# Optimization experiments

Hardware: AMD Instinct MI355X
Metric: run time of the kernel (lower is better)

## Reference

```python
import jax, jax.numpy as jnp
import numpy as np

DIM = 256
HEADS = 8
WS = 8      # window size
SS = 4      # shift size
EPS = 1e-5
HEAD_DIM = DIM // HEADS
SCALE = HEAD_DIM ** (-0.5)
N = WS * WS

# relative position index, replicating tf.meshgrid default 'xy' indexing
_ch = np.arange(WS)
_coords = np.stack(np.meshgrid(_ch, _ch, indexing='xy'))          # [2, WS, WS]
_flat = _coords.reshape(2, -1)                                     # [2, N]
_rel = _flat[:, :, None] - _flat[:, None, :]                       # [2, N, N]
_rel = _rel.transpose(1, 2, 0) + np.array([WS - 1, WS - 1])
_rel = _rel * np.array([2 * WS - 1, 1])
RPI = jnp.asarray(_rel.sum(-1).reshape(-1))                        # [N*N] int


def _calc_mask(H, W):
    # faithful to source: mask is -100 where window region ids are EQUAL, 0 otherwise
    img = np.zeros((H, W))
    slices = (slice(0, -WS), slice(-WS, -SS), slice(-SS, None))
    cnt = 0
    for hs in slices:
        for ws_ in slices:
            img[hs, ws_] = cnt
            cnt += 1
    mw = img.reshape(H // WS, WS, W // WS, WS).transpose(0, 2, 1, 3).reshape(-1, N)
    diff = mw[:, None, :] - mw[:, :, None]
    mask = np.where(diff == 0, -100.0, 0.0).astype(np.float32)     # [nW, N, N]
    return jnp.asarray(mask)


def _layernorm(x, g, b):
    m = jnp.mean(x, axis=-1, keepdims=True)
    v = jnp.mean(jnp.square(x - m), axis=-1, keepdims=True)
    return (x - m) * jax.lax.rsqrt(v + EPS) * g + b


def setup_inputs() -> dict:
    key = jax.random.key(0)
    ks = jax.random.split(key, 8)
    B, L, C = 16, 64 * 64, DIM
    s = 0.02
    return {
        'x': jax.random.normal(ks[0], (B, L, C), jnp.float32),
        'norm1_g': jnp.ones((C,), jnp.float32),
        'norm1_b': jnp.zeros((C,), jnp.float32),
        'qkv_w': jax.random.normal(ks[1], (C, 3 * C), jnp.float32) * s,
        'qkv_b': jnp.zeros((3 * C,), jnp.float32),
        'rpb_table': jax.random.normal(ks[2], ((2 * WS - 1) ** 2, HEADS), jnp.float32) * s,
        'proj_w': jax.random.normal(ks[3], (C, C), jnp.float32) * s,
        'proj_b': jnp.zeros((C,), jnp.float32),
        'norm2_g': jnp.ones((C,), jnp.float32),
        'norm2_b': jnp.zeros((C,), jnp.float32),
        'fc1_w': jax.random.normal(ks[4], (C, 4 * C), jnp.float32) * s,
        'fc1_b': jnp.zeros((4 * C,), jnp.float32),
        'fc2_w': jax.random.normal(ks[5], (4 * C, C), jnp.float32) * s,
        'fc2_b': jnp.zeros((C,), jnp.float32),
        'h': 64,
        'w': 64,
    }


def reference(x, norm1_g, norm1_b, qkv_w, qkv_b, rpb_table, proj_w, proj_b,
              norm2_g, norm2_b, fc1_w, fc1_b, fc2_w, fc2_b, h, w):
    B, L, C = x.shape
    nH, nW = h // WS, w // WS
    nWin = nH * nW
    shortcut = x

    xn = _layernorm(x, norm1_g, norm1_b).reshape(B, h, w, C)
    xn = jnp.roll(xn, shift=(-SS, -SS), axis=(1, 2))                 # cyclic shift
    # window partition -> [B*nWin, N, C]
    xw = xn.reshape(B, nH, WS, nW, WS, C).transpose(0, 1, 3, 2, 4, 5).reshape(B * nWin, N, C)

    qkv = (xw @ qkv_w + qkv_b).reshape(B * nWin, N, 3, HEADS, HEAD_DIM)
    qkv = qkv.transpose(2, 0, 3, 1, 4)                               # [3, B*nWin, H, N, d]
    q, k, v = qkv[0] * SCALE, qkv[1], qkv[2]

    attn = jnp.einsum('bhnd,bhmd->bhnm', q, k)                       # [B*nWin, H, N, N]
    bias = rpb_table[RPI].reshape(N, N, HEADS).transpose(2, 0, 1)    # [H, N, N]
    attn = attn + bias[None]

    mask = _calc_mask(h, w)                                          # [nWin, N, N]
    attn = attn.reshape(B, nWin, HEADS, N, N) + mask[None, :, None]
    attn = jax.nn.softmax(attn, axis=-1).reshape(B * nWin, HEADS, N, N)

    out = jnp.einsum('bhnm,bhmd->bhnd', attn, v)                     # [B*nWin, H, N, d]
    out = out.transpose(0, 2, 1, 3).reshape(B * nWin, N, C)
    out = out @ proj_w + proj_b

    # window reverse + reverse shift
    out = out.reshape(B, nH, nW, WS, WS, C).transpose(0, 1, 3, 2, 4, 5).reshape(B, h, w, C)
    out = jnp.roll(out, shift=(SS, SS), axis=(1, 2)).reshape(B, h * w, C)

    y = shortcut + out
    m = _layernorm(y, norm2_g, norm2_b)
    m = jax.nn.gelu(m @ fc1_w + fc1_b, approximate=False) @ fc2_w + fc2_b
    # faithful to source: final residual reuses the ORIGINAL shortcut, not y
    return shortcut + m
```

## Files before the change

kernel.cpp:

```cpp
#include <hip/hip_runtime.h>
#include <math.h>

typedef __bf16 bf16;
typedef __bf16 bf16x4 __attribute__((ext_vector_type(4)));
typedef __bf16 bf16x8 __attribute__((ext_vector_type(8)));
typedef float f32x4 __attribute__((ext_vector_type(4)));

#define AS1 __attribute__((address_space(1)))
#define AS3 __attribute__((address_space(3)))

__device__ __forceinline__ void gload_lds16(const bf16* g, bf16* l) {
    __builtin_amdgcn_global_load_lds((const AS1 void*)g, (AS3 void*)l, 16, 0, 0);
}

__device__ __forceinline__ float gelu_fast(float v) {
    const float u = 1.5957691216057308f * (v + 0.044715f * v * v * v);
    return v / (1.0f + __expf(-u));
}

__global__ __launch_bounds__(256)
void wprep_all(const float* __restrict__ qkv_w, const float* __restrict__ proj_w,
               const float* __restrict__ fc1_w, const float* __restrict__ fc2_w,
               bf16* __restrict__ qkv_wt, bf16* __restrict__ proj_wt,
               bf16* __restrict__ fc1_wt, bf16* __restrict__ fc2_wt)
{
    int idx = blockIdx.x * 256 + threadIdx.x;
    const float* src; bf16* dst; int K, N;
    if (idx < 196608)            { src = qkv_w;  dst = qkv_wt;  K = 256;  N = 768; }
    else if (idx < 262144)       { idx -= 196608; src = proj_w; dst = proj_wt; K = 256;  N = 256; }
    else if (idx < 524288)       { idx -= 262144; src = fc1_w;  dst = fc1_wt;  K = 256;  N = 1024; }
    else                         { idx -= 524288; src = fc2_w;  dst = fc2_wt;  K = 1024; N = 256; }
    const int k = idx / N, n = idx % N;
    dst[(long)n * K + k] = (bf16)src[idx];
}

__global__ __launch_bounds__(256)
void ln1_window(const float* __restrict__ x, const float* __restrict__ g,
                const float* __restrict__ be, bf16* __restrict__ xw)
{
    const int t = threadIdx.x;
    const int lane = t & 63;
    const int w = t >> 6;
    const long tok = (long)blockIdx.x * 4 + w;
    const float4 v = ((const float4*)(x + tok * 256))[lane];
    float sum = v.x + v.y + v.z + v.w;
    float sq  = v.x * v.x + v.y * v.y + v.z * v.z + v.w * v.w;
#pragma unroll
    for (int m = 32; m >= 1; m >>= 1) {
        sum += __shfl_xor(sum, m, 64);
        sq  += __shfl_xor(sq,  m, 64);
    }
    const float mean = sum * (1.0f / 256.0f);
    const float var  = sq * (1.0f / 256.0f) - mean * mean;
    const float rstd = rsqrtf(var + 1e-5f);
    const float4 gv = ((const float4*)g)[lane];
    const float4 bv = ((const float4*)be)[lane];
    bf16x4 ov;
    ov[0] = (bf16)((v.x - mean) * rstd * gv.x + bv.x);
    ov[1] = (bf16)((v.y - mean) * rstd * gv.y + bv.y);
    ov[2] = (bf16)((v.z - mean) * rstd * gv.z + bv.z);
    ov[3] = (bf16)((v.w - mean) * rstd * gv.w + bv.w);
    const int b = (int)(tok >> 12);
    const int l = (int)(tok & 4095);
    const int i = l >> 6, j = l & 63;
    const int ip = (i + 60) & 63, jp = (j + 60) & 63;
    const int winl = ((ip >> 3) << 3) + (jp >> 3);
    const int n = ((ip & 7) << 3) + (jp & 7);
    const long drow = ((long)b * 64 + winl) * 64 + n;
    *(bf16x4*)(xw + drow * 256 + lane * 4) = ov;
}

__global__ __launch_bounds__(256)
void ln2_kernel(const float* __restrict__ x, const bf16* __restrict__ pj,
                const float* __restrict__ g, const float* __restrict__ be,
                bf16* __restrict__ xn2)
{
    const int t = threadIdx.x;
    const int lane = t & 63;
    const int w = t >> 6;
    const long tok = (long)blockIdx.x * 4 + w;
    const float4 xv = ((const float4*)(x + tok * 256))[lane];
    const bf16x4 pv = *(const bf16x4*)(pj + tok * 256 + lane * 4);
    float y0 = xv.x + (float)pv[0];
    float y1 = xv.y + (float)pv[1];
    float y2 = xv.z + (float)pv[2];
    float y3 = xv.w + (float)pv[3];
    float sum = y0 + y1 + y2 + y3;
    float sq  = y0 * y0 + y1 * y1 + y2 * y2 + y3 * y3;
#pragma unroll
    for (int m = 32; m >= 1; m >>= 1) {
        sum += __shfl_xor(sum, m, 64);
        sq  += __shfl_xor(sq,  m, 64);
    }
    const float mean = sum * (1.0f / 256.0f);
    const float var  = sq * (1.0f / 256.0f) - mean * mean;
    const float rstd = rsqrtf(var + 1e-5f);
    const float4 gv = ((const float4*)g)[lane];
    const float4 bv = ((const float4*)be)[lane];
    bf16x4 ov;
    ov[0] = (bf16)((y0 - mean) * rstd * gv.x + bv.x);
    ov[1] = (bf16)((y1 - mean) * rstd * gv.y + bv.y);
    ov[2] = (bf16)((y2 - mean) * rstd * gv.z + bv.z);
    ov[3] = (bf16)((y3 - mean) * rstd * gv.w + bv.w);
    *(bf16x4*)(xn2 + tok * 256 + lane * 4) = ov;
}

template<int EPI, int KT>
__global__ __launch_bounds__(512, 2)
void gemm_w(const bf16* __restrict__ A, const bf16* __restrict__ Bt,
            const float* __restrict__ bias, void* __restrict__ outp,
            int N, const float* __restrict__ xres, void* __restrict__ aux,
            int gx, int nb)
{
    constexpr int K = KT * 32;
    extern __shared__ bf16 lds[];
    bf16* sA = lds;
    bf16* sB = lds + 3 * 8192;
    const int t = threadIdx.x;
    const int l = t & 63;
    const int w = t >> 6;
    const int wr = w >> 1, wc = w & 1;
    const int q = nb >> 3;
    const int id = ((int)blockIdx.x & 7) * q + ((int)blockIdx.x >> 3);
    const long m0 = (long)(id / gx) * 256;
    const long n0 = (long)(id % gx) * 128;

    const bf16* asrcp[2]; bf16* adstp[2];
#pragma unroll
    for (int j = 0; j < 2; j++) {
        const int idx = j * 512 + t;
        const int p = idx >> 3, s = idx & 7;
        const int sl = s ^ (p & 7);
        const int row = 2 * p + (sl >> 2);
        const int ce = (sl & 3) * 8;
        asrcp[j] = A + (m0 + row) * (long)K + ce;
        adstp[j] = &sA[idx * 8];
    }
    const bf16* bsrcp; bf16* bdstp;
    {
        const int p = t >> 3, s = t & 7;
        const int sl = s ^ (p & 7);
        const int row = 2 * p + (sl >> 2);
        const int ce = (sl & 3) * 8;
        bsrcp = Bt + (n0 + row) * (long)K + ce;
        bdstp = &sB[t * 8];
    }

    const int c = l >> 4;
    int eA[4], eB[4];
#pragma unroll
    for (int i = 0; i < 4; i++) {
        const int rowA = wr * 64 + (l & 15) + i * 16;
        const int pa = rowA >> 1;
        eA[i] = (pa * 8 + ((((rowA & 1) << 2) + c) ^ (pa & 7))) * 8;
        const int rowB = wc * 64 + (l & 15) + i * 16;
        const int pb = rowB >> 1;
        eB[i] = (pb * 8 + ((((rowB & 1) << 2) + c) ^ (pb & 7))) * 8;
    }

    f32x4 acc[4][4];
#pragma unroll
    for (int i = 0; i < 4; i++)
#pragma unroll
        for (int j = 0; j < 4; j++) acc[i][j] = (f32x4){0.f, 0.f, 0.f, 0.f};

#define STAGE(bufi, ko)                                                        \
    do {                                                                       \
        gload_lds16(asrcp[0] + (ko), adstp[0] + (bufi) * 8192);                \
        gload_lds16(asrcp[1] + (ko), adstp[1] + (bufi) * 8192);                \
        gload_lds16(bsrcp + (ko), bdstp + (bufi) * 4096);                      \
    } while (0)

    STAGE(0, 0);
    STAGE(1, 32);

#pragma unroll
    for (int kt = 0; kt < KT; ++kt) {
        const int buf = kt % 3;
        if (kt < KT - 1)
            asm volatile("s_waitcnt vmcnt(3)" ::: "memory");
        else
            asm volatile("s_waitcnt vmcnt(0)" ::: "memory");
        __builtin_amdgcn_s_barrier();
        __builtin_amdgcn_sched_barrier(0);
        if (kt + 2 < KT)
            STAGE((kt + 2) % 3, (kt + 2) * 32);
        bf16x8 av[4], bv[4];
#pragma unroll
        for (int ni = 0; ni < 4; ni++)
            bv[ni] = *(const bf16x8*)&sB[buf * 4096 + eB[ni]];
#pragma unroll
        for (int mi = 0; mi < 4; mi++)
            av[mi] = *(const bf16x8*)&sA[buf * 8192 + eA[mi]];
#pragma unroll
        for (int mi = 0; mi < 4; mi++)
#pragma unroll
            for (int ni = 0; ni < 4; ni++)
                acc[mi][ni] = __builtin_amdgcn_mfma_f32_16x16x32_bf16(
                    bv[ni], av[mi], acc[mi][ni], 0, 0, 0);
    }
#undef STAGE

    const bool transpose_path = (EPI == 2) || (EPI == 0 && n0 < 512);
    if (transpose_path) {
        __syncthreads();
        char* wlds = (char*)(lds) + w * 8704;
#pragma unroll
        for (int mi = 0; mi < 4; mi++)
#pragma unroll
            for (int ni = 0; ni < 4; ni++) {
                const int colb = (ni * 16 + (l >> 4) * 4) * 2;
                const int rowl = mi * 16 + (l & 15);
                const float4 bz = *(const float4*)&bias[n0 + wc * 64 + ni * 16 + (l >> 4) * 4];
                float vv[4];
                vv[0] = acc[mi][ni][0] + bz.x;
                vv[1] = acc[mi][ni][1] + bz.y;
                vv[2] = acc[mi][ni][2] + bz.z;
                vv[3] = acc[mi][ni][3] + bz.w;
                if constexpr (EPI == 2) {
#pragma unroll
                    for (int j = 0; j < 4; j++) vv[j] = gelu_fast(vv[j]);
                }
                bf16x4 ov;
#pragma unroll
                for (int j = 0; j < 4; j++) ov[j] = (bf16)vv[j];
                *(bf16x4*)(wlds + rowl * 136 + (colb ^ ((rowl & 7) << 4))) = ov;
            }
        bf16* outb = (bf16*)outp;
#pragma unroll
        for (int j = 0; j < 8; j++) {
            const int r = j * 8 + (l >> 3);
            const bf16x8 vr = *(const bf16x8*)(wlds + r * 136 + (((l & 7) * 16) ^ ((r & 7) << 4)));
            const long row = m0 + wr * 64 + r;
            const int col = (int)(n0 + wc * 64 + (l & 7) * 8);
            *(bf16x8*)&outb[row * N + col] = vr;
        }
    } else {
#pragma unroll
        for (int mi = 0; mi < 4; mi++)
#pragma unroll
            for (int ni = 0; ni < 4; ni++) {
                const long row = m0 + wr * 64 + mi * 16 + (l & 15);
                const int col = (int)(n0 + wc * 64 + ni * 16 + (l >> 4) * 4);
                const float4 bz = *(const float4*)&bias[col];
                float vv[4];
                vv[0] = acc[mi][ni][0] + bz.x;
                vv[1] = acc[mi][ni][1] + bz.y;
                vv[2] = acc[mi][ni][2] + bz.z;
                vv[3] = acc[mi][ni][3] + bz.w;
                if constexpr (EPI == 3) {
                    const float4 xr = *(const float4*)&xres[row * N + col];
                    float4 ov = {vv[0] + xr.x, vv[1] + xr.y, vv[2] + xr.z, vv[3] + xr.w};
                    *(float4*)&((float*)outp)[row * N + col] = ov;
                } else if constexpr (EPI == 0) {
                    bf16* vt = (bf16*)aux;
                    const int win = (int)(row >> 6);
                    const int n = (int)(row & 63);
#pragma unroll
                    for (int j = 0; j < 4; j++)
                        vt[(long)win * 16384 + (col - 512 + j) * 64 + n] = (bf16)vv[j];
                } else {
                    bf16x4 ov;
#pragma unroll
                    for (int j = 0; j < 4; j++) ov[j] = (bf16)vv[j];
                    if constexpr (EPI == 1) {
                        const int gwin = (int)(row >> 6);
                        const int n = (int)(row & 63);
                        const int bb = gwin >> 6, wi = gwin & 63;
                        const int ipp = ((wi >> 3) << 3) + (n >> 3);
                        const int jpp = ((wi & 7) << 3) + (n & 7);
                        const int ii = (ipp + 4) & 63, jj = (jpp + 4) & 63;
                        const long tok = ((long)bb << 12) + (ii << 6) + jj;
                        *(bf16x4*)&((bf16*)outp)[tok * 256 + col] = ov;
                    } else {
                        *(bf16x4*)&((bf16*)outp)[row * N + col] = ov;
                    }
                }
            }
    }
    (void)xres; (void)aux;
}

__global__ __launch_bounds__(256, 4)
void attn_kernel(const bf16* __restrict__ qkv, const bf16* __restrict__ vT,
                 const float* __restrict__ rpb, bf16* __restrict__ out)
{
    __shared__ bf16 P_lds[4][64 * 64];
    const int t = threadIdx.x;
    const int lane = t & 63;
    const int w = t >> 6;
    const int win = blockIdx.x >> 1;
    const int head = (blockIdx.x & 1) * 4 + w;
    const int wi = win & 63;
    const int lr = lane & 15;
    const int lg = lane >> 4;
    const int lk = lg * 8;
    const long base = (long)win * 64 * 768;
    const float scale = 0.17677669529663687f;
    const int whb = (wi >> 3) << 3;
    const int wwb = (wi & 7) << 3;
    const f32x4 z4 = {0.f, 0.f, 0.f, 0.f};

    const bf16* qp  = qkv + base + head * 32;
    const bf16* kp  = qkv + base + 256 + head * 32;
    const bf16* vtp = vT + (long)win * 16384 + head * 32 * 64;

    int idm[4];
#pragma unroll
    for (int ni = 0; ni < 4; ni++) {
        const int m = ni * 16 + lr;
        const int gi2 = whb + (m >> 3), gj2 = wwb + (m & 7);
        idm[ni] = (gi2 < 56 ? 0 : (gi2 < 60 ? 1 : 2)) * 3 + (gj2 < 56 ? 0 : (gj2 < 60 ? 1 : 2));
    }

    bf16x8 aq[4], bk[4];
#pragma unroll
    for (int mi = 0; mi < 4; mi++)
        aq[mi] = *(const bf16x8*)(qp + (mi * 16 + lr) * 768 + lk);
#pragma unroll
    for (int ni = 0; ni < 4; ni++)
        bk[ni] = *(const bf16x8*)(kp + (ni * 16 + lr) * 768 + lk);

    f32x4 s[4][4];
#pragma unroll
    for (int i = 0; i < 4; i++)
#pragma unroll
        for (int j = 0; j < 4; j++) s[i][j] = z4;
#pragma unroll
    for (int mi = 0; mi < 4; mi++)
#pragma unroll
        for (int ni = 0; ni < 4; ni++)
            s[mi][ni] = __builtin_amdgcn_mfma_f32_16x16x32_bf16(aq[mi], bk[ni], s[mi][ni], 0, 0, 0);

#pragma unroll
    for (int mi = 0; mi < 4; mi++)
#pragma unroll
        for (int r = 0; r < 4; r++) {
            const int n = mi * 16 + lg * 4 + r;
            const int gi = whb + (n >> 3);
            const int gj = wwb + (n & 7);
            const int idn = (gi < 56 ? 0 : (gi < 60 ? 1 : 2)) * 3 + (gj < 56 ? 0 : (gj < 60 ? 1 : 2));
            float vals[4];
            float rowmax = -3.0e38f;
#pragma unroll
            for (int ni = 0; ni < 4; ni++) {
                const int m = ni * 16 + lr;
                const int dj = (n & 7) - (m & 7);
                const int di = (n >> 3) - (m >> 3);
                float sv = s[mi][ni][r] * scale + rpb[((dj + 7) * 15 + (di + 7)) * 8 + head];
                if (idn == idm[ni]) sv -= 100.0f;
                vals[ni] = sv;
                rowmax = fmaxf(rowmax, sv);
            }
#pragma unroll
            for (int msk = 8; msk >= 1; msk >>= 1)
                rowmax = fmaxf(rowmax, __shfl_xor(rowmax, msk, 64));
            float rsum = 0.f;
#pragma unroll
            for (int ni = 0; ni < 4; ni++) {
                const float p = __expf(vals[ni] - rowmax);
                vals[ni] = p;
                rsum += p;
            }
#pragma unroll
            for (int msk = 8; msk >= 1; msk >>= 1)
                rsum += __shfl_xor(rsum, msk, 64);
            const float inv = 1.0f / rsum;
            const int swz = (n & 7) << 3;
#pragma unroll
            for (int ni = 0; ni < 4; ni++)
                P_lds[w][n * 64 + ((ni * 16 + lr) ^ swz)] = (bf16)(vals[ni] * inv);
        }

    f32x4 o[4][2];
#pragma unroll
    for (int i = 0; i < 4; i++)
#pragma unroll
        for (int j = 0; j < 2; j++) o[i][j] = z4;
#pragma unroll
    for (int kk = 0; kk < 2; kk++) {
        bf16x8 bv[2];
#pragma unroll
        for (int ni = 0; ni < 2; ni++)
            bv[ni] = *(const bf16x8*)&vtp[(ni * 16 + lr) * 64 + kk * 32 + lk];
#pragma unroll
        for (int mi = 0; mi < 4; mi++) {
            const int row = mi * 16 + lr;
            const bf16x8 ap = *(const bf16x8*)&P_lds[w][row * 64 + ((kk * 32 + lk) ^ ((row & 7) << 3))];
#pragma unroll
            for (int ni = 0; ni < 2; ni++)
                o[mi][ni] = __builtin_amdgcn_mfma_f32_16x16x32_bf16(bv[ni], ap, o[mi][ni], 0, 0, 0);
        }
    }
#pragma unroll
    for (int mi = 0; mi < 4; mi++)
#pragma unroll
        for (int ni = 0; ni < 2; ni++) {
            const int n = mi * 16 + lr;
            const int d = ni * 16 + lg * 4;
            bf16x4 ov;
            ov[0] = (bf16)o[mi][ni][0]; ov[1] = (bf16)o[mi][ni][1];
            ov[2] = (bf16)o[mi][ni][2]; ov[3] = (bf16)o[mi][ni][3];
            *(bf16x4*)(out + ((long)(win * 64 + n)) * 256 + head * 32 + d) = ov;
        }
}

extern "C" void kernel_launch(void* const* d_in, const int* in_sizes, int n_in,
                              void* d_out, int out_size, void* d_ws, size_t ws_size,
                              hipStream_t stream)
{
    (void)in_sizes; (void)n_in; (void)out_size;
    const float* x      = (const float*)d_in[0];
    const float* n1g    = (const float*)d_in[1];
    const float* n1b    = (const float*)d_in[2];
    const float* qkv_w  = (const float*)d_in[3];
    const float* qkv_b  = (const float*)d_in[4];
    const float* rpb    = (const float*)d_in[5];
    const float* proj_w = (const float*)d_in[6];
    const float* proj_b = (const float*)d_in[7];
    const float* n2g    = (const float*)d_in[8];
    const float* n2b    = (const float*)d_in[9];
    const float* fc1_w  = (const float*)d_in[10];
    const float* fc1_b  = (const float*)d_in[11];
    const float* fc2_w  = (const float*)d_in[12];
    const float* fc2_b  = (const float*)d_in[13];
    float* out = (float*)d_out;

    char* ws = (char*)d_ws;
    bf16* qkv_wt  = (bf16*)(ws + 0);
    bf16* proj_wt = (bf16*)(ws + 393216);
    bf16* fc1_wt  = (bf16*)(ws + 524288);
    bf16* fc2_wt  = (bf16*)(ws + 1048576);
    bf16* xw      = (bf16*)(ws + 2097152);
    bf16* qkvb    = (bf16*)(ws + 35651584);
    bf16* attn_o  = xw;
    bf16* proj_o  = qkvb;
    bf16* vT      = (bf16*)d_out;
    bf16* xn2     = (bf16*)d_out;
    bf16* hbuf    = xw;
    if (ws_size < 136314880ull) return;

    const size_t LB = 73728;

    wprep_all<<<3072, 256, 0, stream>>>(qkv_w, proj_w, fc1_w, fc2_w,
                                        qkv_wt, proj_wt, fc1_wt, fc2_wt);

    ln1_window<<<16384, 256, 0, stream>>>(x, n1g, n1b, xw);
    gemm_w<0, 8><<<1536, 512, LB, stream>>>(xw, qkv_wt, qkv_b, qkvb, 768, nullptr, vT, 6, 1536);
    attn_kernel<<<2048, 256, 0, stream>>>(qkvb, vT, rpb, attn_o);
    gemm_w<1, 8><<<512, 512, LB, stream>>>(attn_o, proj_wt, proj_b, proj_o, 256, nullptr, nullptr, 2, 512);
    ln2_kernel<<<16384, 256, 0, stream>>>(x, proj_o, n2g, n2b, xn2);
    gemm_w<2, 8><<<2048, 512, LB, stream>>>(xn2, fc1_wt, fc1_b, hbuf, 1024, nullptr, nullptr, 8, 2048);
    gemm_w<3, 32><<<512, 512, LB, stream>>>(hbuf, fc2_wt, fc2_b, out, 256, x, nullptr, 2, 512);
}
```

Measured before the change: 284.4 us.

## Fuse fc1+GELU+fc2 MLP into one kernel keeping hidden activations in LDS

```diff
diff --git a/kernel.cpp b/kernel.cpp
--- a/kernel.cpp
+++ b/kernel.cpp
@@ -201,7 +201,7 @@
     }
 #undef STAGE
 
-    const bool transpose_path = (EPI == 2) || (EPI == 0 && n0 < 512);
+    const bool transpose_path = (EPI == 0 && n0 < 512);
     if (transpose_path) {
         __syncthreads();
         char* wlds = (char*)(lds) + w * 8704;
@@ -217,10 +217,6 @@
                 vv[1] = acc[mi][ni][1] + bz.y;
                 vv[2] = acc[mi][ni][2] + bz.z;
                 vv[3] = acc[mi][ni][3] + bz.w;
-                if constexpr (EPI == 2) {
-#pragma unroll
-                    for (int j = 0; j < 4; j++) vv[j] = gelu_fast(vv[j]);
-                }
                 bf16x4 ov;
 #pragma unroll
                 for (int j = 0; j < 4; j++) ov[j] = (bf16)vv[j];
@@ -248,11 +244,7 @@
                 vv[1] = acc[mi][ni][1] + bz.y;
                 vv[2] = acc[mi][ni][2] + bz.z;
                 vv[3] = acc[mi][ni][3] + bz.w;
-                if constexpr (EPI == 3) {
-                    const float4 xr = *(const float4*)&xres[row * N + col];
-                    float4 ov = {vv[0] + xr.x, vv[1] + xr.y, vv[2] + xr.z, vv[3] + xr.w};
-                    *(float4*)&((float*)outp)[row * N + col] = ov;
-                } else if constexpr (EPI == 0) {
+                if constexpr (EPI == 0) {
                     bf16* vt = (bf16*)aux;
                     const int win = (int)(row >> 6);
                     const int n = (int)(row & 63);
@@ -263,22 +255,208 @@
                     bf16x4 ov;
 #pragma unroll
                     for (int j = 0; j < 4; j++) ov[j] = (bf16)vv[j];
-                    if constexpr (EPI == 1) {
-                        const int gwin = (int)(row >> 6);
-                        const int n = (int)(row & 63);
-                        const int bb = gwin >> 6, wi = gwin & 63;
-                        const int ipp = ((wi >> 3) << 3) + (n >> 3);
-                        const int jpp = ((wi & 7) << 3) + (n & 7);
-                        const int ii = (ipp + 4) & 63, jj = (jpp + 4) & 63;
-                        const long tok = ((long)bb << 12) + (ii << 6) + jj;
-                        *(bf16x4*)&((bf16*)outp)[tok * 256 + col] = ov;
-                    } else {
-                        *(bf16x4*)&((bf16*)outp)[row * N + col] = ov;
-                    }
+                    const int gwin = (int)(row >> 6);
+                    const int n = (int)(row & 63);
+                    const int bb = gwin >> 6, wi = gwin & 63;
+                    const int ipp = ((wi >> 3) << 3) + (n >> 3);
+                    const int jpp = ((wi & 7) << 3) + (n & 7);
+                    const int ii = (ipp + 4) & 63, jj = (jpp + 4) & 63;
+                    const long tok = ((long)bb << 12) + (ii << 6) + jj;
+                    *(bf16x4*)&((bf16*)outp)[tok * 256 + col] = ov;
                 }
             }
     }
     (void)xres; (void)aux;
+}
+
+__global__ __launch_bounds__(512, 2)
+void fused_mlp(const bf16* __restrict__ xn2, const bf16* __restrict__ w1t,
+               const bf16* __restrict__ w2t, const float* __restrict__ b1,
+               const float* __restrict__ b2, const float* __restrict__ xres,
+               float* __restrict__ out, int nb)
+{
+    extern __shared__ bf16 lds[];
+    bf16* sX = lds;
+    bf16* sW = lds + 32768;
+    char* sH = (char*)(lds + 32768 + 24576);
+    const int t = threadIdx.x;
+    const int l = t & 63;
+    const int w = t >> 6;
+    const int wr = w >> 2, wc = w & 3;
+    const int q = nb >> 3;
+    const int id = ((int)blockIdx.x & 7) * q + ((int)blockIdx.x >> 3);
+    const long m0 = (long)id * 128;
+
+    const bf16* w1base; bf16* w1dst;
+    {
+        const int p = t >> 3, s = t & 7;
+        const int sl = s ^ (p & 7);
+        const int row = 2 * p + (sl >> 2);
+        const int ce = (sl & 3) * 8;
+        w1base = w1t + (long)row * 256 + ce;
+        w1dst = sW + t * 8;
+    }
+    const bf16* w2base[2]; bf16* w2dst[2];
+#pragma unroll
+    for (int j = 0; j < 2; j++) {
+        const int cc = j * 512 + t;
+        const int p = cc >> 3, s = cc & 7;
+        const int sl = s ^ (p & 7);
+        const int row = 2 * p + (sl >> 2);
+        const int ce = (sl & 3) * 8;
+        w2base[j] = w2t + (long)row * 1024 + ce;
+        w2dst[j] = sW + cc * 8;
+    }
+
+    const int c = l >> 4;
+    int eXA[4], eB1[2], eB2[4], hrA[4], hwOf[4][2];
+#pragma unroll
+    for (int i = 0; i < 4; i++) {
+        const int row = wr * 64 + i * 16 + (l & 15);
+        const int p = row >> 1;
+        eXA[i] = (p * 8 + ((((row & 1) << 2) + c) ^ (p & 7))) * 8;
+        hrA[i] = row * 272 + c * 16;
+#pragma unroll
+        for (int nj = 0; nj < 2; nj++)
+            hwOf[i][nj] = row * 272 + (wc * 32 + nj * 16 + (l >> 4) * 4) * 2;
+    }
+#pragma unroll
+    for (int nj = 0; nj < 2; nj++) {
+        const int brow = wc * 32 + nj * 16 + (l & 15);
+        const int p = brow >> 1;
+        eB1[nj] = (p * 8 + ((((brow & 1) << 2) + c) ^ (p & 7))) * 8;
+    }
+#pragma unroll
+    for (int nj = 0; nj < 4; nj++) {
+        const int brow = wc * 64 + nj * 16 + (l & 15);
+        const int p = brow >> 1;
+        eB2[nj] = (p * 8 + ((((brow & 1) << 2) + c) ^ (p & 7))) * 8;
+    }
+
+    {
+#pragma unroll
+        for (int j = 0; j < 8; j++) {
+            const int idx = j * 512 + t;
+            const int kt = idx >> 9, cc = idx & 511;
+            const int p = cc >> 3, s = cc & 7;
+            const int sl = s ^ (p & 7);
+            const int row = 2 * p + (sl >> 2);
+            const int ce = (sl & 3) * 8;
+            gload_lds16(xn2 + (m0 + row) * 256 + kt * 32 + ce, sX + kt * 4096 + cc * 8);
+        }
+    }
+#define STAGE_P1(hc_, kt_, buf_) \
+    gload_lds16(w1base + (hc_) * 32768 + (kt_) * 32, w1dst + (buf_) * 8192)
+#define STAGE_P2(hc_, kt2_, buf_)                                              \
+    do {                                                                       \
+        gload_lds16(w2base[0] + (hc_) * 128 + (kt2_) * 32, w2dst[0] + (buf_) * 8192); \
+        gload_lds16(w2base[1] + (hc_) * 128 + (kt2_) * 32, w2dst[1] + (buf_) * 8192); \
+    } while (0)
+#define STAGE_G(g_)                                                            \
+    do {                                                                       \
+        if ((g_) < 96) {                                                       \
+            if (((g_) % 12) < 8) STAGE_P1((g_) / 12, (g_) % 12, (g_) % 3);     \
+            else STAGE_P2((g_) / 12, (g_) % 12 - 8, (g_) % 3);                 \
+        }                                                                      \
+    } while (0)
+#define PIPE_WAIT(gn_)                                                         \
+    do {                                                                       \
+        if ((gn_) >= 96)                                                       \
+            asm volatile("s_waitcnt vmcnt(0) lgkmcnt(0)" ::: "memory");        \
+        else if (((gn_) % 12) < 8)                                             \
+            asm volatile("s_waitcnt vmcnt(1) lgkmcnt(0)" ::: "memory");        \
+        else                                                                   \
+            asm volatile("s_waitcnt vmcnt(2) lgkmcnt(0)" ::: "memory");        \
+    } while (0)
+
+    STAGE_P1(0, 0, 0);
+    STAGE_P1(0, 1, 1);
+
+    f32x4 acc[4][4];
+#pragma unroll
+    for (int i = 0; i < 4; i++)
+#pragma unroll
+        for (int j = 0; j < 4; j++) acc[i][j] = (f32x4){0.f, 0.f, 0.f, 0.f};
+
+#pragma unroll
+    for (int hc = 0; hc < 8; hc++) {
+        f32x4 acc1[4][2];
+#pragma unroll
+        for (int i = 0; i < 4; i++)
+#pragma unroll
+            for (int j = 0; j < 2; j++) acc1[i][j] = (f32x4){0.f, 0.f, 0.f, 0.f};
+
+#pragma unroll
+        for (int kt = 0; kt < 8; kt++) {
+            const int g = hc * 12 + kt;
+            PIPE_WAIT(g + 1);
+            __builtin_amdgcn_s_barrier();
+            __builtin_amdgcn_sched_barrier(0);
+            STAGE_G(g + 2);
+            const int buf = g % 3;
+            bf16x8 b0 = *(const bf16x8*)&sW[buf * 8192 + eB1[0]];
+            bf16x8 b1 = *(const bf16x8*)&sW[buf * 8192 + eB1[1]];
+#pragma unroll
+            for (int mi = 0; mi < 4; mi++) {
+                const bf16x8 av = *(const bf16x8*)&sX[kt * 4096 + eXA[mi]];
+                acc1[mi][0] = __builtin_amdgcn_mfma_f32_16x16x32_bf16(b0, av, acc1[mi][0], 0, 0, 0);
+                acc1[mi][1] = __builtin_amdgcn_mfma_f32_16x16x32_bf16(b1, av, acc1[mi][1], 0, 0, 0);
+            }
+        }
+#pragma unroll
+        for (int mi = 0; mi < 4; mi++)
+#pragma unroll
+            for (int nj = 0; nj < 2; nj++) {
+                const int hcol = wc * 32 + nj * 16 + (l >> 4) * 4;
+                const float4 bz = *(const float4*)&b1[hc * 128 + hcol];
+                bf16x4 hv;
+                hv[0] = (bf16)gelu_fast(acc1[mi][nj][0] + bz.x);
+                hv[1] = (bf16)gelu_fast(acc1[mi][nj][1] + bz.y);
+                hv[2] = (bf16)gelu_fast(acc1[mi][nj][2] + bz.z);
+                hv[3] = (bf16)gelu_fast(acc1[mi][nj][3] + bz.w);
+                *(bf16x4*)(sH + hwOf[mi][nj]) = hv;
+            }
+#pragma unroll
+        for (int kt2 = 0; kt2 < 4; kt2++) {
+            const int g = hc * 12 + 8 + kt2;
+            PIPE_WAIT(g + 1);
+            __builtin_amdgcn_s_barrier();
+            __builtin_amdgcn_sched_barrier(0);
+            STAGE_G(g + 2);
+            const int buf = g % 3;
+            bf16x8 bb[4];
+#pragma unroll
+            for (int nj = 0; nj < 4; nj++)
+                bb[nj] = *(const bf16x8*)&sW[buf * 8192 + eB2[nj]];
+#pragma unroll
+            for (int mi = 0; mi < 4; mi++) {
+                const bf16x8 av = *(const bf16x8*)(sH + hrA[mi] + kt2 * 64);
+#pragma unroll
+                for (int nj = 0; nj < 4; nj++)
+                    acc[mi][nj] = __builtin_amdgcn_mfma_f32_16x16x32_bf16(bb[nj], av, acc[mi][nj], 0, 0, 0);
+            }
+        }
+    }
+#undef STAGE_P1
+#undef STAGE_P2
+#undef STAGE_G
+#undef PIPE_WAIT
+
+#pragma unroll
+    for (int mi = 0; mi < 4; mi++)
+#pragma unroll
+        for (int nj = 0; nj < 4; nj++) {
+            const long row = m0 + wr * 64 + mi * 16 + (l & 15);
+            const int col = wc * 64 + nj * 16 + (l >> 4) * 4;
+            const float4 bz = *(const float4*)&b2[col];
+            const float4 xr = *(const float4*)&xres[row * 256 + col];
+            float4 ov;
+            ov.x = acc[mi][nj][0] + bz.x + xr.x;
+            ov.y = acc[mi][nj][1] + bz.y + xr.y;
+            ov.z = acc[mi][nj][2] + bz.z + xr.z;
+            ov.w = acc[mi][nj][3] + bz.w + xr.w;
+            *(float4*)&out[row * 256 + col] = ov;
+        }
 }
 
 __global__ __launch_bounds__(256, 4)
@@ -436,11 +614,11 @@
     bf16* attn_o  = xw;
     bf16* proj_o  = qkvb;
     bf16* vT      = (bf16*)d_out;
-    bf16* xn2     = (bf16*)d_out;
-    bf16* hbuf    = xw;
+    bf16* xn2     = xw;
     if (ws_size < 136314880ull) return;
 
-    const size_t LB = 73728;
+    const size_t LB  = 73728;
+    const size_t LBM = 149504;
 
     wprep_all<<<3072, 256, 0, stream>>>(qkv_w, proj_w, fc1_w, fc2_w,
                                         qkv_wt, proj_wt, fc1_wt, fc2_wt);
@@ -450,6 +628,5 @@
     attn_kernel<<<2048, 256, 0, stream>>>(qkvb, vT, rpb, attn_o);
     gemm_w<1, 8><<<512, 512, LB, stream>>>(attn_o, proj_wt, proj_b, proj_o, 256, nullptr, nullptr, 2, 512);
     ln2_kernel<<<16384, 256, 0, stream>>>(x, proj_o, n2g, n2b, xn2);
-    gemm_w<2, 8><<<2048, 512, LB, stream>>>(xn2, fc1_wt, fc1_b, hbuf, 1024, nullptr, nullptr, 8, 2048);
-    gemm_w<3, 32><<<512, 512, LB, stream>>>(hbuf, fc2_wt, fc2_b, out, 256, x, nullptr, 2, 512);
-}
+    fused_mlp<<<512, 512, LBM, stream>>>(xn2, fc1_wt, fc2_wt, fc1_b, fc2_b, x, out, 512);
+}
```

Result: slower. 331.4 us (+16.5%).

## Fuse projection GEMM with residual add and LayerNorm2 into one kernel

Applied to the files above, without the earlier changes.

```diff
diff --git a/kernel.cpp b/kernel.cpp
--- a/kernel.cpp
+++ b/kernel.cpp
@@ -68,41 +68,6 @@
     const int n = ((ip & 7) << 3) + (jp & 7);
     const long drow = ((long)b * 64 + winl) * 64 + n;
     *(bf16x4*)(xw + drow * 256 + lane * 4) = ov;
-}
-
-__global__ __launch_bounds__(256)
-void ln2_kernel(const float* __restrict__ x, const bf16* __restrict__ pj,
-                const float* __restrict__ g, const float* __restrict__ be,
-                bf16* __restrict__ xn2)
-{
-    const int t = threadIdx.x;
-    const int lane = t & 63;
-    const int w = t >> 6;
-    const long tok = (long)blockIdx.x * 4 + w;
-    const float4 xv = ((const float4*)(x + tok * 256))[lane];
-    const bf16x4 pv = *(const bf16x4*)(pj + tok * 256 + lane * 4);
-    float y0 = xv.x + (float)pv[0];
-    float y1 = xv.y + (float)pv[1];
-    float y2 = xv.z + (float)pv[2];
-    float y3 = xv.w + (float)pv[3];
-    float sum = y0 + y1 + y2 + y3;
-    float sq  = y0 * y0 + y1 * y1 + y2 * y2 + y3 * y3;
-#pragma unroll
-    for (int m = 32; m >= 1; m >>= 1) {
-        sum += __shfl_xor(sum, m, 64);
-        sq  += __shfl_xor(sq,  m, 64);
-    }
-    const float mean = sum * (1.0f / 256.0f);
-    const float var  = sq * (1.0f / 256.0f) - mean * mean;
-    const float rstd = rsqrtf(var + 1e-5f);
-    const float4 gv = ((const float4*)g)[lane];
-    const float4 bv = ((const float4*)be)[lane];
-    bf16x4 ov;
-    ov[0] = (bf16)((y0 - mean) * rstd * gv.x + bv.x);
-    ov[1] = (bf16)((y1 - mean) * rstd * gv.y + bv.y);
-    ov[2] = (bf16)((y2 - mean) * rstd * gv.z + bv.z);
-    ov[3] = (bf16)((y3 - mean) * rstd * gv.w + bv.w);
-    *(bf16x4*)(xn2 + tok * 256 + lane * 4) = ov;
 }
 
 template<int EPI, int KT>
@@ -259,26 +224,175 @@
 #pragma unroll
                     for (int j = 0; j < 4; j++)
                         vt[(long)win * 16384 + (col - 512 + j) * 64 + n] = (bf16)vv[j];
-                } else {
-                    bf16x4 ov;
-#pragma unroll
-                    for (int j = 0; j < 4; j++) ov[j] = (bf16)vv[j];
-                    if constexpr (EPI == 1) {
-                        const int gwin = (int)(row >> 6);
-                        const int n = (int)(row & 63);
-                        const int bb = gwin >> 6, wi = gwin & 63;
-                        const int ipp = ((wi >> 3) << 3) + (n >> 3);
-                        const int jpp = ((wi & 7) << 3) + (n & 7);
-                        const int ii = (ipp + 4) & 63, jj = (jpp + 4) & 63;
-                        const long tok = ((long)bb << 12) + (ii << 6) + jj;
-                        *(bf16x4*)&((bf16*)outp)[tok * 256 + col] = ov;
-                    } else {
-                        *(bf16x4*)&((bf16*)outp)[row * N + col] = ov;
-                    }
                 }
             }
     }
     (void)xres; (void)aux;
+}
+
+__global__ __launch_bounds__(512, 2)
+void proj_ln2(const bf16* __restrict__ A, const bf16* __restrict__ Bt,
+              const float* __restrict__ bias, const float* __restrict__ x,
+              const float* __restrict__ g2, const float* __restrict__ b2,
+              bf16* __restrict__ xn2, int nb)
+{
+    extern __shared__ bf16 lds[];
+    bf16* sA = lds;
+    bf16* sB = lds + 3 * 4096;
+    float* sred = (float*)(lds + 3 * 4096 + 3 * 8192);
+    const int t = threadIdx.x;
+    const int l = t & 63;
+    const int w = t >> 6;
+    const int wr = w >> 2, wc = w & 3;
+    const int q = nb >> 3;
+    const int id = ((int)blockIdx.x & 7) * q + ((int)blockIdx.x >> 3);
+    const long m0 = (long)id * 128;
+
+    const bf16* asrcp; bf16* adstp;
+    {
+        const int p = t >> 3, s = t & 7;
+        const int sl = s ^ (p & 7);
+        const int row = 2 * p + (sl >> 2);
+        const int ce = (sl & 3) * 8;
+        asrcp = A + (m0 + row) * 256 + ce;
+        adstp = &sA[t * 8];
+    }
+    const bf16* bsrcp[2]; bf16* bdstp[2];
+#pragma unroll
+    for (int j = 0; j < 2; j++) {
+        const int idx = j * 512 + t;
+        const int p = idx >> 3, s = idx & 7;
+        const int sl = s ^ (p & 7);
+        const int row = 2 * p + (sl >> 2);
+        const int ce = (sl & 3) * 8;
+        bsrcp[j] = Bt + (long)row * 256 + ce;
+        bdstp[j] = &sB[idx * 8];
+    }
+
+    const int c = l >> 4;
+    int eA[4], eB[4];
+#pragma unroll
+    for (int i = 0; i < 4; i++) {
+        const int rowA = wr * 64 + (l & 15) + i * 16;
+        const int pa = rowA >> 1;
+        eA[i] = (pa * 8 + ((((rowA & 1) << 2) + c) ^ (pa & 7))) * 8;
+        const int rowB = wc * 64 + (l & 15) + i * 16;
+        const int pb = rowB >> 1;
+        eB[i] = (pb * 8 + ((((rowB & 1) << 2) + c) ^ (pb & 7))) * 8;
+    }
+
+    f32x4 acc[4][4];
+#pragma unroll
+    for (int i = 0; i < 4; i++)
+#pragma unroll
+        for (int j = 0; j < 4; j++) acc[i][j] = (f32x4){0.f, 0.f, 0.f, 0.f};
+
+#define STAGE(bufi, ko)                                                        \
+    do {                                                                       \
+        gload_lds16(asrcp + (ko), adstp + (bufi) * 4096);                      \
+        gload_lds16(bsrcp[0] + (ko), bdstp[0] + (bufi) * 8192);                \
+        gload_lds16(bsrcp[1] + (ko), bdstp[1] + (bufi) * 8192);                \
+    } while (0)
+
+    STAGE(0, 0);
+    STAGE(1, 32);
+
+#pragma unroll
+    for (int kt = 0; kt < 8; ++kt) {
+        const int buf = kt % 3;
+        if (kt < 7)
+            asm volatile("s_waitcnt vmcnt(3)" ::: "memory");
+        else
+            asm volatile("s_waitcnt vmcnt(0)" ::: "memory");
+        __builtin_amdgcn_s_barrier();
+        __builtin_amdgcn_sched_barrier(0);
+        if (kt + 2 < 8)
+            STAGE((kt + 2) % 3, (kt + 2) * 32);
+        bf16x8 av[4], bv[4];
+#pragma unroll
+        for (int ni = 0; ni < 4; ni++)
+            bv[ni] = *(const bf16x8*)&sB[buf * 8192 + eB[ni]];
+#pragma unroll
+        for (int mi = 0; mi < 4; mi++)
+            av[mi] = *(const bf16x8*)&sA[buf * 4096 + eA[mi]];
+#pragma unroll
+        for (int mi = 0; mi < 4; mi++)
+#pragma unroll
+            for (int ni = 0; ni < 4; ni++)
+                acc[mi][ni] = __builtin_amdgcn_mfma_f32_16x16x32_bf16(
+                    bv[ni], av[mi], acc[mi][ni], 0, 0, 0);
+    }
+#undef STAGE
+
+    float ts[4] = {0.f, 0.f, 0.f, 0.f}, tq[4] = {0.f, 0.f, 0.f, 0.f};
+    long tok[4];
+#pragma unroll
+    for (int mi = 0; mi < 4; mi++) {
+        const long row = m0 + wr * 64 + mi * 16 + (l & 15);
+        const int gwin = (int)(row >> 6);
+        const int n = (int)(row & 63);
+        const int bb = gwin >> 6, wi = gwin & 63;
+        const int ipp = ((wi >> 3) << 3) + (n >> 3);
+        const int jpp = ((wi & 7) << 3) + (n & 7);
+        const int ii = (ipp + 4) & 63, jj = (jpp + 4) & 63;
+        tok[mi] = ((long)bb << 12) + (ii << 6) + jj;
+#pragma unroll
+        for (int ni = 0; ni < 4; ni++) {
+            const int col = wc * 64 + ni * 16 + (l >> 4) * 4;
+            const float4 bz = *(const float4*)&bias[col];
+            const float4 xr = *(const float4*)&x[tok[mi] * 256 + col];
+            acc[mi][ni][0] += bz.x + xr.x;
+            acc[mi][ni][1] += bz.y + xr.y;
+            acc[mi][ni][2] += bz.z + xr.z;
+            acc[mi][ni][3] += bz.w + xr.w;
+#pragma unroll
+            for (int j = 0; j < 4; j++) {
+                ts[mi] += acc[mi][ni][j];
+                tq[mi] += acc[mi][ni][j] * acc[mi][ni][j];
+            }
+        }
+    }
+#pragma unroll
+    for (int mi = 0; mi < 4; mi++) {
+        ts[mi] += __shfl_xor(ts[mi], 16, 64);
+        tq[mi] += __shfl_xor(tq[mi], 16, 64);
+        ts[mi] += __shfl_xor(ts[mi], 32, 64);
+        tq[mi] += __shfl_xor(tq[mi], 32, 64);
+    }
+    if (l < 16) {
+#pragma unroll
+        for (int mi = 0; mi < 4; mi++) {
+            const int r = wr * 64 + mi * 16 + l;
+            sred[r * 9 + wc * 2]     = ts[mi];
+            sred[r * 9 + wc * 2 + 1] = tq[mi];
+        }
+    }
+    __syncthreads();
+#pragma unroll
+    for (int mi = 0; mi < 4; mi++) {
+        const int r = wr * 64 + mi * 16 + (l & 15);
+        float S = 0.f, Q = 0.f;
+#pragma unroll
+        for (int k = 0; k < 4; k++) {
+            S += sred[r * 9 + k * 2];
+            Q += sred[r * 9 + k * 2 + 1];
+        }
+        const float mean = S * (1.0f / 256.0f);
+        const float var  = Q * (1.0f / 256.0f) - mean * mean;
+        const float rstd = rsqrtf(var + 1e-5f);
+#pragma unroll
+        for (int ni = 0; ni < 4; ni++) {
+            const int col = wc * 64 + ni * 16 + (l >> 4) * 4;
+            const float4 gg = *(const float4*)&g2[col];
+            const float4 bb = *(const float4*)&b2[col];
+            bf16x4 ov;
+            ov[0] = (bf16)((acc[mi][ni][0] - mean) * rstd * gg.x + bb.x);
+            ov[1] = (bf16)((acc[mi][ni][1] - mean) * rstd * gg.y + bb.y);
+            ov[2] = (bf16)((acc[mi][ni][2] - mean) * rstd * gg.z + bb.z);
+            ov[3] = (bf16)((acc[mi][ni][3] - mean) * rstd * gg.w + bb.w);
+            *(bf16x4*)&xn2[tok[mi] * 256 + col] = ov;
+        }
+    }
 }
 
 __global__ __launch_bounds__(256, 4)
@@ -434,13 +548,13 @@
     bf16* xw      = (bf16*)(ws + 2097152);
     bf16* qkvb    = (bf16*)(ws + 35651584);
     bf16* attn_o  = xw;
-    bf16* proj_o  = qkvb;
     bf16* vT      = (bf16*)d_out;
-    bf16* xn2     = (bf16*)d_out;
+    bf16* xn2     = (bf16*)d_out + 16777216;
     bf16* hbuf    = xw;
     if (ws_size < 136314880ull) return;
 
-    const size_t LB = 73728;
+    const size_t LB  = 73728;
+    const size_t LBP = 78336;
 
     wprep_all<<<3072, 256, 0, stream>>>(qkv_w, proj_w, fc1_w, fc2_w,
                                         qkv_wt, proj_wt, fc1_wt, fc2_wt);
@@ -448,8 +562,7 @@
     ln1_window<<<16384, 256, 0, stream>>>(x, n1g, n1b, xw);
     gemm_w<0, 8><<<1536, 512, LB, stream>>>(xw, qkv_wt, qkv_b, qkvb, 768, nullptr, vT, 6, 1536);
     attn_kernel<<<2048, 256, 0, stream>>>(qkvb, vT, rpb, attn_o);
-    gemm_w<1, 8><<<512, 512, LB, stream>>>(attn_o, proj_wt, proj_b, proj_o, 256, nullptr, nullptr, 2, 512);
-    ln2_kernel<<<16384, 256, 0, stream>>>(x, proj_o, n2g, n2b, xn2);
+    proj_ln2<<<512, 512, LBP, stream>>>(attn_o, proj_wt, proj_b, x, n2g, n2b, xn2, 512);
     gemm_w<2, 8><<<2048, 512, LB, stream>>>(xn2, fc1_wt, fc1_b, hbuf, 1024, nullptr, nullptr, 8, 2048);
     gemm_w<3, 32><<<512, 512, LB, stream>>>(hbuf, fc2_wt, fc2_b, out, 256, x, nullptr, 2, 512);
 }
```

Result: no change. 281.4 us (-1.1%).
